# Kernel tuning notes

Measured on AMD Instinct MI355X. Metric: run time of the kernel, lower is better.

The kernel has to match this reference:

```python
import jax, jax.numpy as jnp
import numpy as np

VOC = 32000
D = 512          # embedding_dim == hidden_dim
POS = 1024       # position_embeddings_count


def _layernorm(x, gamma, beta, eps=1e-5):
    mu = jnp.mean(x, axis=-1, keepdims=True)
    var = jnp.var(x, axis=-1, keepdims=True)
    return (x - mu) * jax.lax.rsqrt(var + eps) * gamma + beta


def setup_inputs() -> dict:
    key = jax.random.key(0)
    ks = jax.random.split(key, 7)
    inp = jax.random.randint(ks[0], (32, 1024), 0, VOC)
    word_emb = jax.random.normal(ks[1], (VOC, D), dtype=jnp.float32) * 0.02
    pos_emb = jax.random.normal(ks[2], (POS, D), dtype=jnp.float32) * 0.02
    gamma = jnp.ones((D,), dtype=jnp.float32)
    beta = jnp.zeros((D,), dtype=jnp.float32)
    # torch.rand -> uniform [0,1) init in the original Attention module
    Wk = jax.random.uniform(ks[3], (D, D), dtype=jnp.float32)
    Wq = jax.random.uniform(ks[4], (D, D), dtype=jnp.float32)
    Wv = jax.random.uniform(ks[5], (D, D), dtype=jnp.float32)
    return {"input": inp, "word_emb": word_emb, "pos_emb": pos_emb,
            "gamma": gamma, "beta": beta, "Wk": Wk, "Wq": Wq, "Wv": Wv}


def reference(input, word_emb, pos_emb, gamma, beta, Wk, Wq, Wv):
    S = input.shape[-1]
    # MiniBertEmbedding: word + positional, then LayerNorm
    emb = word_emb[input] + pos_emb[:S][None, :, :]   # [B,S,D]
    x = _layernorm(emb, gamma, beta)
    # Attention: single-head QK^T softmax V with param matrices
    k = jnp.einsum('bsd,dh->bsh', x, Wk)
    q = jnp.einsum('bsd,dh->bsh', x, Wq)
    v = jnp.einsum('bsd,do->bso', x, Wv)
    qk = jnp.einsum('bqh,bkh->bqk', q, k) / jnp.sqrt(jnp.float32(D))
    attn = jax.nn.softmax(qk, axis=-1)
    return jnp.einsum('bqk,bko->bqo', attn, v)
```

## Files before the change

### kernel.cpp

```cpp
#include <hip/hip_runtime.h>
#include <math.h>

typedef _Float16 f16;
typedef _Float16 half8 __attribute__((ext_vector_type(8)));
typedef _Float16 hv2 __attribute__((ext_vector_type(2)));
typedef _Float16 hv4 __attribute__((ext_vector_type(4)));
typedef float f32x4 __attribute__((ext_vector_type(4)));
typedef __attribute__((address_space(1))) const unsigned int gu32;
typedef __attribute__((address_space(3))) unsigned int lu32;

#define BB 32
#define SS 1024
#define DD 512
#define NR (BB*SS)
#define CH 16

__device__ __forceinline__ void stage128(const char* g, int ldb, char* lds,
                                         int wv, int ln) {
  #pragma unroll
  for (int r = 0; r < 4; r++) {
    int slot = r * 256 + wv * 64 + ln;
    int row = slot >> 3, cp = slot & 7;
    int c = cp ^ (row & 7);
    const char* gp = g + (size_t)row * ldb + (c << 4);
    char* lp = lds + ((slot - ln) << 4);
    __builtin_amdgcn_global_load_lds((gu32*)gp, (lu32*)lp, 16, 0, 0);
  }
}

__device__ __forceinline__ void stage8k_512(const char* g, int ldb, char* lds) {
  int tid = threadIdx.x;
  int slot = tid;
  int row = slot >> 3, cp = slot & 7;
  int c = cp ^ (row & 7);
  const char* gp = g + (size_t)row * ldb + (c << 4);
  char* lp = lds + ((slot - (tid & 63)) << 4);
  __builtin_amdgcn_global_load_lds((gu32*)gp, (lu32*)lp, 16, 0, 0);
}

__device__ __forceinline__ void stage16k_512(const char* g, int ldb, char* lds) {
  int tid = threadIdx.x;
  #pragma unroll
  for (int r = 0; r < 2; r++) {
    int slot = r * 512 + tid;
    int row = slot >> 3, cp = slot & 7;
    int c = cp ^ (row & 7);
    const char* gp = g + (size_t)row * ldb + (c << 4);
    char* lp = lds + ((slot - (tid & 63)) << 4);
    __builtin_amdgcn_global_load_lds((gu32*)gp, (lu32*)lp, 16, 0, 0);
  }
}

__device__ __forceinline__ half8 frag_ld(const char* lds, int row, int kc) {
  return *(const half8*)(lds + row * 128 + ((kc ^ (row & 7)) << 4));
}

__device__ __forceinline__ f32x4 MF(half8 a, half8 b, f32x4 c) {
  return __builtin_amdgcn_mfma_f32_16x16x32_f16(a, b, c, 0, 0, 0);
}

__global__ __launch_bounds__(256) void k_prep(
    const int* __restrict__ inp, const float* __restrict__ wemb,
    const float* __restrict__ pemb, const float* __restrict__ gamma,
    const float* __restrict__ beta, f16* __restrict__ Xhi, f16* __restrict__ Xlo,
    const float* __restrict__ Wq, const float* __restrict__ Wk,
    const float* __restrict__ Wv, f16* __restrict__ Wqh, f16* __restrict__ Wql,
    f16* __restrict__ Wkh, f16* __restrict__ Wkl, f16* __restrict__ Wvt)
{
  int bid = blockIdx.x;
  int tid = threadIdx.x;
  __shared__ float red[10];
  __shared__ float Lt[64][65];
  if (bid >= NR) {
    int t  = bid - NR;
    int mz = t >> 6;
    int tt = t & 63;
    if (mz < 2) {
      const float* W = mz ? Wk : Wq;
      f16* Oh = mz ? Wkh : Wqh;
      f16* Ol = mz ? Wkl : Wql;
      #pragma unroll
      for (int p = 0; p < 4; p++) {
        size_t base = (size_t)tt * 4096 + p * 1024 + tid * 4;
        float4 v = *(const float4*)&W[base];
        f16 h0 = (f16)v.x, h1 = (f16)v.y, h2 = (f16)v.z, h3 = (f16)v.w;
        hv4 hi = {h0, h1, h2, h3};
        hv4 lo = {(f16)(v.x - (float)h0), (f16)(v.y - (float)h1),
                  (f16)(v.z - (float)h2), (f16)(v.w - (float)h3)};
        *(hv4*)&Oh[base] = hi;
        *(hv4*)&Ol[base] = lo;
      }
      return;
    }
    int tr = tt >> 3, tc = tt & 7;
    int rr = tid >> 4;
    int c4 = (tid & 15) * 4;
    #pragma unroll
    for (int p = 0; p < 4; p++) {
      float4 v = *(const float4*)&Wv[(size_t)(tr * 64 + p * 16 + rr) * DD + tc * 64 + c4];
      Lt[p * 16 + rr][c4 + 0] = v.x; Lt[p * 16 + rr][c4 + 1] = v.y;
      Lt[p * 16 + rr][c4 + 2] = v.z; Lt[p * 16 + rr][c4 + 3] = v.w;
    }
    __syncthreads();
    #pragma unroll
    for (int p = 0; p < 4; p++) {
      int dl = p * 16 + rr;
      float v0 = Lt[c4 + 0][dl], v1 = Lt[c4 + 1][dl];
      float v2 = Lt[c4 + 2][dl], v3 = Lt[c4 + 3][dl];
      size_t o = (size_t)(tc * 64 + dl) * DD + tr * 64 + c4;
      *(hv4*)&Wvt[o] = (hv4){(f16)v0, (f16)v1, (f16)v2, (f16)v3};
    }
    return;
  }
  int row = bid;
  int s   = row & (SS - 1);
  int tok = inp[row];
  float2 w = ((const float2*)(wemb + (size_t)tok * DD))[tid];
  float2 p = ((const float2*)(pemb + (size_t)s   * DD))[tid];
  float ex = w.x + p.x, ey = w.y + p.y;
  float sum = ex + ey, ssq = ex*ex + ey*ey;
  #pragma unroll
  for (int off = 32; off > 0; off >>= 1) {
    sum += __shfl_down(sum, off, 64);
    ssq += __shfl_down(ssq, off, 64);
  }
  int wv = tid >> 6, ln = tid & 63;
  if (ln == 0) { red[wv] = sum; red[4 + wv] = ssq; }
  __syncthreads();
  if (tid == 0) {
    float s4 = red[0] + red[1] + red[2] + red[3];
    float q4 = red[4] + red[5] + red[6] + red[7];
    float mean = s4 * (1.0f / DD);
    float var  = q4 * (1.0f / DD) - mean * mean;
    red[8] = mean; red[9] = rsqrtf(var + 1e-5f);
  }
  __syncthreads();
  float mean = red[8], rstd = red[9];
  float2 g  = ((const float2*)gamma)[tid];
  float2 bt = ((const float2*)beta)[tid];
  float ox = (ex - mean) * rstd * g.x + bt.x;
  float oy = (ey - mean) * rstd * g.y + bt.y;
  f16 hx = (f16)ox, hy = (f16)oy;
  f16 lx = (f16)(ox - (float)hx), ly = (f16)(oy - (float)hy);
  ((hv2*)(Xhi + (size_t)row * DD))[tid] = (hv2){hx, hy};
  ((hv2*)(Xlo + (size_t)row * DD))[tid] = (hv2){lx, ly};
}

__global__ __launch_bounds__(256, 2) void k_mt(
    const f16* __restrict__ Wkh, const f16* __restrict__ Wkl,
    const f16* __restrict__ Wqh, const f16* __restrict__ Wql,
    f16* __restrict__ Mthi, f16* __restrict__ Mtlo)
{
  __shared__ __align__(16) char Ah[16384], Al[16384], Bh[16384], Bl[16384];
  int tid = threadIdx.x, wv = tid >> 6, ln = tid & 63;
  int mw = wv & 1, nw = wv >> 1;
  int n0 = blockIdx.x * 128;
  int m0 = blockIdx.y * 128;
  f32x4 acc[4][4];
  #pragma unroll
  for (int i = 0; i < 4; i++)
    #pragma unroll
    for (int j = 0; j < 4; j++) acc[i][j] = (f32x4)(0.0f);
  int quad = ln >> 4, l15 = ln & 15;
  for (int k0 = 0; k0 < DD; k0 += 64) {
    __syncthreads();
    stage128((const char*)(Wkh + (size_t)m0 * DD + k0), 1024, Ah, wv, ln);
    stage128((const char*)(Wkl + (size_t)m0 * DD + k0), 1024, Al, wv, ln);
    stage128((const char*)(Wqh + (size_t)n0 * DD + k0), 1024, Bh, wv, ln);
    stage128((const char*)(Wql + (size_t)n0 * DD + k0), 1024, Bl, wv, ln);
    __syncthreads();
    #pragma unroll
    for (int ks = 0; ks < 2; ks++) {
      int kc = ks * 4 + quad;
      half8 ah[4], al[4], bh[4], bl[4];
      #pragma unroll
      for (int t = 0; t < 4; t++) {
        ah[t] = frag_ld(Ah, mw * 64 + t * 16 + l15, kc);
        al[t] = frag_ld(Al, mw * 64 + t * 16 + l15, kc);
        bh[t] = frag_ld(Bh, nw * 64 + t * 16 + l15, kc);
        bl[t] = frag_ld(Bl, nw * 64 + t * 16 + l15, kc);
      }
      #pragma unroll
      for (int i = 0; i < 4; i++)
        #pragma unroll
        for (int j = 0; j < 4; j++) {
          acc[i][j] = MF(ah[i], bh[j], acc[i][j]);
          acc[i][j] = MF(ah[i], bl[j], acc[i][j]);
          acc[i][j] = MF(al[i], bh[j], acc[i][j]);
        }
    }
  }
  #pragma unroll
  for (int i = 0; i < 4; i++)
    #pragma unroll
    for (int j = 0; j < 4; j++)
      #pragma unroll
      for (int rg = 0; rg < 4; rg++) {
        int gm = m0 + mw * 64 + i * 16 + quad * 4 + rg;
        int gn = n0 + nw * 64 + j * 16 + l15;
        size_t o = (size_t)gm * DD + gn;
        float v = acc[i][j][rg];
        f16 h = (f16)v;
        Mthi[o] = h; Mtlo[o] = (f16)(v - (float)h);
      }
}

__global__ __launch_bounds__(512, 4) void k_projm(
    const f16* __restrict__ Xhi, const f16* __restrict__ Xlo,
    const f16* __restrict__ Mthi, const f16* __restrict__ Mtlo,
    f16* __restrict__ Sqhi, f16* __restrict__ Sqlo)
{
  __shared__ __align__(16) char Ah[16384], Al[16384], Bh[16384], Bl[16384];
  int tid = threadIdx.x, wv = tid >> 6, ln = tid & 63;
  int mw = wv & 1, nw = wv >> 1;
  int L = blockIdx.x;
  int xb = (L >> 3) & 3;
  int y  = ((L >> 5) << 3) + (L & 7);
  int n0 = xb * 128;
  int m0 = y * 128;
  f32x4 acc[4][2];
  #pragma unroll
  for (int i = 0; i < 4; i++)
    #pragma unroll
    for (int j = 0; j < 2; j++) acc[i][j] = (f32x4)(0.0f);
  int quad = ln >> 4, l15 = ln & 15;
  for (int k0 = 0; k0 < DD; k0 += 64) {
    __syncthreads();
    stage16k_512((const char*)(Xhi  + (size_t)m0 * DD + k0), 1024, Ah);
    stage16k_512((const char*)(Xlo  + (size_t)m0 * DD + k0), 1024, Al);
    stage16k_512((const char*)(Mthi + (size_t)n0 * DD + k0), 1024, Bh);
    stage16k_512((const char*)(Mtlo + (size_t)n0 * DD + k0), 1024, Bl);
    __syncthreads();
    #pragma unroll
    for (int ks = 0; ks < 2; ks++) {
      int kc = ks * 4 + quad;
      half8 ah[4], al[4], bh[2], bl[2];
      #pragma unroll
      for (int t = 0; t < 4; t++) {
        ah[t] = frag_ld(Ah, mw * 64 + t * 16 + l15, kc);
        al[t] = frag_ld(Al, mw * 64 + t * 16 + l15, kc);
      }
      #pragma unroll
      for (int t = 0; t < 2; t++) {
        bh[t] = frag_ld(Bh, nw * 32 + t * 16 + l15, kc);
        bl[t] = frag_ld(Bl, nw * 32 + t * 16 + l15, kc);
      }
      #pragma unroll
      for (int i = 0; i < 4; i++)
        #pragma unroll
        for (int j = 0; j < 2; j++) {
          acc[i][j] = MF(ah[i], bh[j], acc[i][j]);
          acc[i][j] = MF(ah[i], bl[j], acc[i][j]);
          acc[i][j] = MF(al[i], bh[j], acc[i][j]);
        }
    }
  }
  #pragma unroll
  for (int i = 0; i < 4; i++)
    #pragma unroll
    for (int j = 0; j < 2; j++)
      #pragma unroll
      for (int rg = 0; rg < 4; rg++) {
        int gm = m0 + mw * 64 + i * 16 + quad * 4 + rg;
        int gn = n0 + nw * 32 + j * 16 + l15;
        size_t o = (size_t)gm * DD + gn;
        float v = acc[i][j][rg];
        f16 h = (f16)v;
        Sqhi[o] = h; Sqlo[o] = (f16)(v - (float)h);
      }
}

__global__ __launch_bounds__(256, 2) void k_vt(
    const f16* __restrict__ Wvt, const f16* __restrict__ Xhi, f16* __restrict__ Vt)
{
  __shared__ __align__(16) char Ah[2][16384], Bh[2][16384];
  int tid = threadIdx.x, wv = tid >> 6, ln = tid & 63;
  int mw = wv & 1, nw = wv >> 1;
  int orig = blockIdx.x;
  int L = (orig & 7) * 128 + (orig >> 3);
  int c = L >> 7, t = L & 127;
  int m0 = (t & 3) * 128;
  int n0 = (c * 32 + (t >> 2)) * 128;
  f32x4 acc[4][4];
  #pragma unroll
  for (int i = 0; i < 4; i++)
    #pragma unroll
    for (int j = 0; j < 4; j++) acc[i][j] = (f32x4)(0.0f);
  int quad = ln >> 4, l15 = ln & 15;
  stage128((const char*)(Wvt + (size_t)m0 * DD), 1024, Ah[0], wv, ln);
  stage128((const char*)(Xhi + (size_t)n0 * DD), 1024, Bh[0], wv, ln);
  for (int k0 = 0; k0 < DD; k0 += 64) {
    int cur = (k0 >> 6) & 1;
    __builtin_amdgcn_s_barrier();
    __builtin_amdgcn_sched_barrier(0);
    if (k0 + 64 < DD) {
      stage128((const char*)(Wvt + (size_t)m0 * DD + k0 + 64), 1024, Ah[cur ^ 1], wv, ln);
      stage128((const char*)(Xhi + (size_t)n0 * DD + k0 + 64), 1024, Bh[cur ^ 1], wv, ln);
      asm volatile("s_waitcnt vmcnt(8)" ::: "memory");
    } else {
      asm volatile("s_waitcnt vmcnt(0)" ::: "memory");
    }
    __builtin_amdgcn_s_barrier();
    __builtin_amdgcn_sched_barrier(0);
    #pragma unroll
    for (int ks = 0; ks < 2; ks++) {
      int kc = ks * 4 + quad;
      half8 a[4], b[4];
      #pragma unroll
      for (int tt = 0; tt < 4; tt++) {
        a[tt] = frag_ld(Ah[cur], mw * 64 + tt * 16 + l15, kc);
        b[tt] = frag_ld(Bh[cur], nw * 64 + tt * 16 + l15, kc);
      }
      #pragma unroll
      for (int i = 0; i < 4; i++)
        #pragma unroll
        for (int j = 0; j < 4; j++) acc[i][j] = MF(a[i], b[j], acc[i][j]);
    }
  }
  #pragma unroll
  for (int i = 0; i < 4; i++)
    #pragma unroll
    for (int j = 0; j < 4; j++)
      #pragma unroll
      for (int rg = 0; rg < 4; rg++) {
        int gm = m0 + mw * 64 + i * 16 + quad * 4 + rg;
        int gn = n0 + nw * 64 + j * 16 + l15;
        Vt[(size_t)gm * NR + gn] = (f16)acc[i][j][rg];
      }
}

__global__ __launch_bounds__(512, 2) void k_qk(
    const f16* __restrict__ Sqhi, const f16* __restrict__ Sqlo,
    const f16* __restrict__ Xhi, const f16* __restrict__ Xlo,
    f16* __restrict__ Pws, f16* __restrict__ Pd)
{
  __shared__ __align__(16) char Ah[8192], Al[8192];
  __shared__ __align__(16) char Bh[2][4][8192], Bl[2][4][8192];
  __shared__ float redm[4][64], reds[4][64];
  int tid = threadIdx.x, wv = tid >> 6, ln = tid & 63;
  int rowg = wv & 1, qd = wv >> 1;
  int L = blockIdx.x;
  int g  = L >> 7;
  int rr = L & 127;
  int z  = g * 8 + (rr & 7);
  int m0 = (rr >> 3) * 64;
  size_t zr = (size_t)z * SS;
  f32x4 acc[2][16];
  #pragma unroll
  for (int i = 0; i < 2; i++)
    #pragma unroll
    for (int j = 0; j < 16; j++) acc[i][j] = (f32x4)(0.0f);
  int quad = ln >> 4, l15 = ln & 15;

  stage8k_512((const char*)(Sqhi + (zr + m0) * DD), 1024, Ah);
  stage8k_512((const char*)(Sqlo + (zr + m0) * DD), 1024, Al);
  #pragma unroll
  for (int q4 = 0; q4 < 4; q4++) {
    stage8k_512((const char*)(Xhi + (zr + q4 * 256) * DD), 1024, Bh[0][q4]);
    stage8k_512((const char*)(Xlo + (zr + q4 * 256) * DD), 1024, Bl[0][q4]);
  }

  half8 afh[2][2], afl[2][2];
  for (int k0 = 0; k0 < DD; k0 += 64) {
    #pragma unroll
    for (int r = 0; r < 4; r++) {
      __builtin_amdgcn_s_barrier();
      __builtin_amdgcn_sched_barrier(0);
      bool lastPhase = (k0 == DD - 64 && r == 3);
      if (!lastPhase) {
        int nk0 = (r == 3) ? k0 + 64 : k0;
        int nr  = (r + 1) & 3;
        #pragma unroll
        for (int q4 = 0; q4 < 4; q4++) {
          int n0 = q4 * 256 + nr * 64;
          stage8k_512((const char*)(Xhi + (zr + n0) * DD + nk0), 1024, Bh[(r + 1) & 1][q4]);
          stage8k_512((const char*)(Xlo + (zr + n0) * DD + nk0), 1024, Bl[(r + 1) & 1][q4]);
        }
        if (r == 3) {
          stage8k_512((const char*)(Sqhi + (zr + m0) * DD + k0 + 64), 1024, Ah);
          stage8k_512((const char*)(Sqlo + (zr + m0) * DD + k0 + 64), 1024, Al);
          asm volatile("s_waitcnt vmcnt(10)" ::: "memory");
        } else {
          asm volatile("s_waitcnt vmcnt(8)" ::: "memory");
        }
      } else {
        asm volatile("s_waitcnt vmcnt(0)" ::: "memory");
      }
      __builtin_amdgcn_s_barrier();
      __builtin_amdgcn_sched_barrier(0);
      if (r == 0) {
        #pragma unroll
        for (int ks = 0; ks < 2; ks++)
          #pragma unroll
          for (int i = 0; i < 2; i++) {
            afh[ks][i] = frag_ld(Ah, rowg * 32 + i * 16 + l15, ks * 4 + quad);
            afl[ks][i] = frag_ld(Al, rowg * 32 + i * 16 + l15, ks * 4 + quad);
          }
      }
      #pragma unroll
      for (int ks = 0; ks < 2; ks++) {
        int kc = ks * 4 + quad;
        #pragma unroll
        for (int jj = 0; jj < 4; jj++) {
          half8 bh = frag_ld(Bh[r & 1][qd], jj * 16 + l15, kc);
          half8 bl = frag_ld(Bl[r & 1][qd], jj * 16 + l15, kc);
          #pragma unroll
          for (int i = 0; i < 2; i++) {
            acc[i][r * 4 + jj] = MF(afh[ks][i], bh, acc[i][r * 4 + jj]);
            acc[i][r * 4 + jj] = MF(afh[ks][i], bl, acc[i][r * 4 + jj]);
            acc[i][r * 4 + jj] = MF(afl[ks][i], bh, acc[i][r * 4 + jj]);
          }
        }
      }
    }
  }

  const float scale = 0.044194173824159216f;
  float mx[2][4];
  #pragma unroll
  for (int i = 0; i < 2; i++)
    #pragma unroll
    for (int rg = 0; rg < 4; rg++) mx[i][rg] = -3.0e38f;
  #pragma unroll
  for (int i = 0; i < 2; i++)
    #pragma unroll
    for (int j = 0; j < 16; j++)
      #pragma unroll
      for (int rg = 0; rg < 4; rg++) {
        acc[i][j][rg] *= scale;
        mx[i][rg] = fmaxf(mx[i][rg], acc[i][j][rg]);
      }
  #pragma unroll
  for (int off = 1; off < 16; off <<= 1)
    #pragma unroll
    for (int i = 0; i < 2; i++)
      #pragma unroll
      for (int rg = 0; rg < 4; rg++)
        mx[i][rg] = fmaxf(mx[i][rg], __shfl_xor(mx[i][rg], off, 64));
  if (l15 == 0) {
    #pragma unroll
    for (int i = 0; i < 2; i++)
      #pragma unroll
      for (int rg = 0; rg < 4; rg++)
        redm[qd][rowg * 32 + i * 16 + quad * 4 + rg] = mx[i][rg];
  }
  __syncthreads();
  float fm[2][4], sum[2][4];
  #pragma unroll
  for (int i = 0; i < 2; i++)
    #pragma unroll
    for (int rg = 0; rg < 4; rg++) {
      int row = rowg * 32 + i * 16 + quad * 4 + rg;
      fm[i][rg] = fmaxf(fmaxf(redm[0][row], redm[1][row]),
                        fmaxf(redm[2][row], redm[3][row]));
      sum[i][rg] = 0.0f;
    }
  #pragma unroll
  for (int i = 0; i < 2; i++)
    #pragma unroll
    for (int j = 0; j < 16; j++)
      #pragma unroll
      for (int rg = 0; rg < 4; rg++) {
        float e = __expf(acc[i][j][rg] - fm[i][rg]);
        acc[i][j][rg] = e;
        sum[i][rg] += e;
      }
  #pragma unroll
  for (int off = 1; off < 16; off <<= 1)
    #pragma unroll
    for (int i = 0; i < 2; i++)
      #pragma unroll
      for (int rg = 0; rg < 4; rg++)
        sum[i][rg] += __shfl_xor(sum[i][rg], off, 64);
  if (l15 == 0) {
    #pragma unroll
    for (int i = 0; i < 2; i++)
      #pragma unroll
      for (int rg = 0; rg < 4; rg++)
        reds[qd][rowg * 32 + i * 16 + quad * 4 + rg] = sum[i][rg];
  }
  __syncthreads();
  float inv[2][4];
  #pragma unroll
  for (int i = 0; i < 2; i++)
    #pragma unroll
    for (int rg = 0; rg < 4; rg++) {
      int row = rowg * 32 + i * 16 + quad * 4 + rg;
      inv[i][rg] = 1.0f / (reds[0][row] + reds[1][row] + reds[2][row] + reds[3][row]);
    }
  f16* Pb = (z < CH) ? Pws : Pd;
  size_t zo = (size_t)((z < CH) ? z : z - CH);
  #pragma unroll
  for (int i = 0; i < 2; i++)
    #pragma unroll
    for (int j = 0; j < 16; j++)
      #pragma unroll
      for (int rg = 0; rg < 4; rg++) {
        int row = rowg * 32 + i * 16 + quad * 4 + rg;
        int col = qd * 256 + j * 16 + l15;
        Pb[(zo * SS + m0 + row) * SS + col] = (f16)(acc[i][j][rg] * inv[i][rg]);
      }
}

__global__ __launch_bounds__(256, 2) void k_pv(
    const f16* __restrict__ P, const f16* __restrict__ Vt, float* __restrict__ O,
    int zoff)
{
  __shared__ __align__(16) char Ah[2][16384], Bh[2][16384];
  int tid = threadIdx.x, wv = tid >> 6, ln = tid & 63;
  int mw = wv & 1, nw = wv >> 1;
  int orig = blockIdx.x;
  int L = (orig & 7) * 64 + (orig >> 3);
  int c = L >> 6, t = L & 63;
  int zl = 2 * c + (t >> 5);
  int m0 = ((t >> 2) & 7) * 128;
  int n0 = (t & 3) * 128;
  int b  = zoff + zl;
  const char* Pt = (const char*)(P + ((size_t)zl * SS + m0) * SS);
  const char* Vb = (const char*)(Vt + (size_t)n0 * NR + (size_t)b * SS);
  f32x4 acc[4][4];
  #pragma unroll
  for (int i = 0; i < 4; i++)
    #pragma unroll
    for (int j = 0; j < 4; j++) acc[i][j] = (f32x4)(0.0f);
  int quad = ln >> 4, l15 = ln & 15;
  stage128(Pt, 2048, Ah[0], wv, ln);
  stage128(Vb, NR * 2, Bh[0], wv, ln);
  for (int k0 = 0; k0 < SS; k0 += 64) {
    int cur = (k0 >> 6) & 1;
    __builtin_amdgcn_s_barrier();
    __builtin_amdgcn_sched_barrier(0);
    if (k0 + 64 < SS) {
      stage128(Pt + (k0 + 64) * 2, 2048, Ah[cur ^ 1], wv, ln);
      stage128(Vb + (k0 + 64) * 2, NR * 2, Bh[cur ^ 1], wv, ln);
      asm volatile("s_waitcnt vmcnt(8)" ::: "memory");
    } else {
      asm volatile("s_waitcnt vmcnt(0)" ::: "memory");
    }
    __builtin_amdgcn_s_barrier();
    __builtin_amdgcn_sched_barrier(0);
    #pragma unroll
    for (int ks = 0; ks < 2; ks++) {
      int kc = ks * 4 + quad;
      half8 a[4], bf[4];
      #pragma unroll
      for (int tt = 0; tt < 4; tt++) {
        a[tt]  = frag_ld(Ah[cur], mw * 64 + tt * 16 + l15, kc);
        bf[tt] = frag_ld(Bh[cur], nw * 64 + tt * 16 + l15, kc);
      }
      #pragma unroll
      for (int i = 0; i < 4; i++)
        #pragma unroll
        for (int j = 0; j < 4; j++) acc[i][j] = MF(a[i], bf[j], acc[i][j]);
    }
  }
  #pragma unroll
  for (int i = 0; i < 4; i++)
    #pragma unroll
    for (int j = 0; j < 4; j++)
      #pragma unroll
      for (int rg = 0; rg < 4; rg++) {
        int gm = m0 + mw * 64 + i * 16 + quad * 4 + rg;
        int gn = n0 + nw * 64 + j * 16 + l15;
        O[((size_t)b * SS + gm) * DD + gn] = acc[i][j][rg];
      }
}

extern "C" void kernel_launch(void* const* d_in, const int* in_sizes, int n_in,
                              void* d_out, int out_size, void* d_ws, size_t ws_size,
                              hipStream_t stream) {
  const int*   inp   = (const int*)d_in[0];
  const float* wemb  = (const float*)d_in[1];
  const float* pemb  = (const float*)d_in[2];
  const float* gamma = (const float*)d_in[3];
  const float* beta  = (const float*)d_in[4];
  const float* Wk    = (const float*)d_in[5];
  const float* Wq    = (const float*)d_in[6];
  const float* Wv    = (const float*)d_in[7];

  char* ws = (char*)d_ws;
  f16* Xhi  = (f16*)ws;
  f16* Xlo  = (f16*)(ws + ((size_t)32 << 20));
  f16* Sqhi = (f16*)(ws + ((size_t)64 << 20));
  f16* Sqlo = (f16*)(ws + ((size_t)96 << 20));
  f16* Vt   = (f16*)(ws + ((size_t)128 << 20));
  f16* Pws  = (f16*)(ws + ((size_t)160 << 20));
  f16* Pd   = (f16*)d_out;

  f16* Wqh  = (f16*)d_out;
  f16* Wql  = Wqh + (size_t)DD * DD;
  f16* Wkh  = Wql + (size_t)DD * DD;
  f16* Wkl  = Wkh + (size_t)DD * DD;
  f16* Wvt  = Wkl + (size_t)DD * DD;
  f16* Mthi = Wvt + (size_t)DD * DD;
  f16* Mtlo = Mthi + (size_t)DD * DD;

  k_prep<<<NR + 192, 256, 0, stream>>>(inp, wemb, pemb, gamma, beta, Xhi, Xlo,
                                       Wq, Wk, Wv, Wqh, Wql, Wkh, Wkl, Wvt);
  k_mt<<<dim3(DD / 128, DD / 128), 256, 0, stream>>>(Wkh, Wkl, Wqh, Wql, Mthi, Mtlo);
  k_projm<<<1024, 512, 0, stream>>>(Xhi, Xlo, Mthi, Mtlo, Sqhi, Sqlo);
  k_vt<<<1024, 256, 0, stream>>>(Wvt, Xhi, Vt);
  k_qk<<<512, 512, 0, stream>>>(Sqhi, Sqlo, Xhi, Xlo, Pws, Pd);
  k_pv<<<512, 256, 0, stream>>>(Pd,  Vt, (float*)d_out, CH);
  k_pv<<<512, 256, 0, stream>>>(Pws, Vt, (float*)d_out, 0);
}
```

Baseline: 423.2 us.

## Halve k_qk B-tile LDS staging to 32-row phases and raise occupancy bound

New measurement: 677.2 us. 1.6x slower.

```diff
diff --git a/kernel.cpp b/kernel.cpp
--- a/kernel.cpp
+++ b/kernel.cpp
@@ -46,6 +46,24 @@
     int row = slot >> 3, cp = slot & 7;
     int c = cp ^ (row & 7);
     const char* gp = g + (size_t)row * ldb + (c << 4);
+    char* lp = lds + ((slot - (tid & 63)) << 4);
+    __builtin_amdgcn_global_load_lds((gu32*)gp, (lu32*)lp, 16, 0, 0);
+  }
+}
+
+__device__ __forceinline__ void stageB32(const f16* X, size_t rowbase, int k0,
+                                         char* Bset) {
+  int tid = threadIdx.x;
+  int q4 = tid >> 7;
+  int inner = tid & 127;
+  char* lds = Bset + q4 * 4096;
+  const char* g = (const char*)(X + (rowbase + (size_t)q4 * 256) * DD + k0);
+  #pragma unroll
+  for (int r = 0; r < 2; r++) {
+    int slot = r * 128 + inner;
+    int row = slot >> 3, cp = slot & 7;
+    int c = cp ^ (row & 7);
+    const char* gp = g + (size_t)row * 1024 + (c << 4);
     char* lp = lds + ((slot - (tid & 63)) << 4);
     __builtin_amdgcn_global_load_lds((gu32*)gp, (lu32*)lp, 16, 0, 0);
   }
@@ -329,14 +347,13 @@
       }
 }
 
-__global__ __launch_bounds__(512, 2) void k_qk(
+__global__ __launch_bounds__(512, 4) void k_qk(
     const f16* __restrict__ Sqhi, const f16* __restrict__ Sqlo,
     const f16* __restrict__ Xhi, const f16* __restrict__ Xlo,
     f16* __restrict__ Pws, f16* __restrict__ Pd)
 {
   __shared__ __align__(16) char Ah[8192], Al[8192];
-  __shared__ __align__(16) char Bh[2][4][8192], Bl[2][4][8192];
-  __shared__ float redm[4][64], reds[4][64];
+  __shared__ __align__(16) char Bh[2][16384], Bl[2][16384];
   int tid = threadIdx.x, wv = tid >> 6, ln = tid & 63;
   int rowg = wv & 1, qd = wv >> 1;
   int L = blockIdx.x;
@@ -354,34 +371,27 @@
 
   stage8k_512((const char*)(Sqhi + (zr + m0) * DD), 1024, Ah);
   stage8k_512((const char*)(Sqlo + (zr + m0) * DD), 1024, Al);
-  #pragma unroll
-  for (int q4 = 0; q4 < 4; q4++) {
-    stage8k_512((const char*)(Xhi + (zr + q4 * 256) * DD), 1024, Bh[0][q4]);
-    stage8k_512((const char*)(Xlo + (zr + q4 * 256) * DD), 1024, Bl[0][q4]);
-  }
+  stageB32(Xhi, zr + 0, 0, Bh[0]);
+  stageB32(Xlo, zr + 0, 0, Bl[0]);
 
   half8 afh[2][2], afl[2][2];
   for (int k0 = 0; k0 < DD; k0 += 64) {
     #pragma unroll
-    for (int r = 0; r < 4; r++) {
+    for (int r = 0; r < 8; r++) {
       __builtin_amdgcn_s_barrier();
       __builtin_amdgcn_sched_barrier(0);
-      bool lastPhase = (k0 == DD - 64 && r == 3);
+      bool lastPhase = (k0 == DD - 64 && r == 7);
       if (!lastPhase) {
-        int nk0 = (r == 3) ? k0 + 64 : k0;
-        int nr  = (r + 1) & 3;
-        #pragma unroll
-        for (int q4 = 0; q4 < 4; q4++) {
-          int n0 = q4 * 256 + nr * 64;
-          stage8k_512((const char*)(Xhi + (zr + n0) * DD + nk0), 1024, Bh[(r + 1) & 1][q4]);
-          stage8k_512((const char*)(Xlo + (zr + n0) * DD + nk0), 1024, Bl[(r + 1) & 1][q4]);
-        }
-        if (r == 3) {
+        int nk0 = (r == 7) ? k0 + 64 : k0;
+        int nr  = (r + 1) & 7;
+        stageB32(Xhi, zr + nr * 32, nk0, Bh[(r + 1) & 1]);
+        stageB32(Xlo, zr + nr * 32, nk0, Bl[(r + 1) & 1]);
+        if (r == 7) {
           stage8k_512((const char*)(Sqhi + (zr + m0) * DD + k0 + 64), 1024, Ah);
           stage8k_512((const char*)(Sqlo + (zr + m0) * DD + k0 + 64), 1024, Al);
-          asm volatile("s_waitcnt vmcnt(10)" ::: "memory");
+          asm volatile("s_waitcnt vmcnt(6)" ::: "memory");
         } else {
-          asm volatile("s_waitcnt vmcnt(8)" ::: "memory");
+          asm volatile("s_waitcnt vmcnt(4)" ::: "memory");
         }
       } else {
         asm volatile("s_waitcnt vmcnt(0)" ::: "memory");
@@ -397,23 +407,28 @@
             afl[ks][i] = frag_ld(Al, rowg * 32 + i * 16 + l15, ks * 4 + quad);
           }
       }
+      const char* Bhc = Bh[r & 1] + qd * 4096;
+      const char* Blc = Bl[r & 1] + qd * 4096;
       #pragma unroll
       for (int ks = 0; ks < 2; ks++) {
         int kc = ks * 4 + quad;
         #pragma unroll
-        for (int jj = 0; jj < 4; jj++) {
-          half8 bh = frag_ld(Bh[r & 1][qd], jj * 16 + l15, kc);
-          half8 bl = frag_ld(Bl[r & 1][qd], jj * 16 + l15, kc);
+        for (int jj = 0; jj < 2; jj++) {
+          half8 bh = frag_ld(Bhc, jj * 16 + l15, kc);
+          half8 bl = frag_ld(Blc, jj * 16 + l15, kc);
           #pragma unroll
           for (int i = 0; i < 2; i++) {
-            acc[i][r * 4 + jj] = MF(afh[ks][i], bh, acc[i][r * 4 + jj]);
-            acc[i][r * 4 + jj] = MF(afh[ks][i], bl, acc[i][r * 4 + jj]);
-            acc[i][r * 4 + jj] = MF(afl[ks][i], bh, acc[i][r * 4 + jj]);
+            acc[i][r * 2 + jj] = MF(afh[ks][i], bh, acc[i][r * 2 + jj]);
+            acc[i][r * 2 + jj] = MF(afh[ks][i], bl, acc[i][r * 2 + jj]);
+            acc[i][r * 2 + jj] = MF(afl[ks][i], bh, acc[i][r * 2 + jj]);
           }
         }
       }
     }
   }
+  __syncthreads();
+  float* redm = (float*)&Bh[0][0];
+  float* reds = redm + 256;
 
   const float scale = 0.044194173824159216f;
   float mx[2][4];
@@ -442,7 +457,7 @@
     for (int i = 0; i < 2; i++)
       #pragma unroll
       for (int rg = 0; rg < 4; rg++)
-        redm[qd][rowg * 32 + i * 16 + quad * 4 + rg] = mx[i][rg];
+        redm[qd * 64 + rowg * 32 + i * 16 + quad * 4 + rg] = mx[i][rg];
   }
   __syncthreads();
   float fm[2][4], sum[2][4];
@@ -451,8 +466,8 @@
     #pragma unroll
     for (int rg = 0; rg < 4; rg++) {
       int row = rowg * 32 + i * 16 + quad * 4 + rg;
-      fm[i][rg] = fmaxf(fmaxf(redm[0][row], redm[1][row]),
-                        fmaxf(redm[2][row], redm[3][row]));
+      fm[i][rg] = fmaxf(fmaxf(redm[row], redm[64 + row]),
+                        fmaxf(redm[128 + row], redm[192 + row]));
       sum[i][rg] = 0.0f;
     }
   #pragma unroll
@@ -477,7 +492,7 @@
     for (int i = 0; i < 2; i++)
       #pragma unroll
       for (int rg = 0; rg < 4; rg++)
-        reds[qd][rowg * 32 + i * 16 + quad * 4 + rg] = sum[i][rg];
+        reds[qd * 64 + rowg * 32 + i * 16 + quad * 4 + rg] = sum[i][rg];
   }
   __syncthreads();
   float inv[2][4];
@@ -486,7 +501,7 @@
     #pragma unroll
     for (int rg = 0; rg < 4; rg++) {
       int row = rowg * 32 + i * 16 + quad * 4 + rg;
-      inv[i][rg] = 1.0f / (reds[0][row] + reds[1][row] + reds[2][row] + reds[3][row]);
+      inv[i][rg] = 1.0f / (reds[row] + reds[64 + row] + reds[128 + row] + reds[192 + row]);
     }
   f16* Pb = (z < CH) ? Pws : Pd;
   size_t zo = (size_t)((z < CH) ? z : z - CH);
```
